# Performance work log

Hardware: AMD Instinct MI355X
Metric: run time of the kernel (lower is better)

Reference implementation:

```python
import jax, jax.numpy as jnp
import numpy as np

B, C, H, Wd = 4, 64, 64, 64


def setup_inputs() -> dict:
    key = jax.random.key(0)
    k1, k2, k3 = jax.random.split(key, 3)
    x = jax.random.normal(k1, (B, C, H, Wd), dtype=jnp.float32)
    W = jax.random.normal(k2, (C, C), dtype=jnp.float32) * (1.0 / np.sqrt(C))
    b = jax.random.normal(k3, (C,), dtype=jnp.float32) * 0.01
    return {"x": x, "W": W, "b": b}


def reference(x, W, b):
    Bz, Cz, Hz, Wz = x.shape
    N = Hz * Wz
    xf = x.reshape(Bz, Cz, N)                      # values [B,C,N]
    # shared 1x1 conv for queries and keys (same module instance in torch)
    qk = jnp.einsum('oc,bcn->bon', W, xf) + b[None, :, None]  # [B,C,N]
    # scores[b,n,m] = sum_c q[b,c,n] * k[b,c,m], scaled by 1/N
    scores = jnp.einsum('bcn,bcm->bnm', qk, qk) / N           # [B,N,N]
    attn = jax.nn.softmax(scores, axis=-1)                    # softmax over m
    # out[b,c,n] = sum_m values[b,c,m] * attn[b,n,m]
    out = jnp.einsum('bcm,bnm->bcn', xf, attn)
    return out.reshape(Bz, Cz, Hz, Wz)
```

## Files before the change

kernel.cpp:

```cpp
#include <hip/hip_runtime.h>
#include <hip/hip_bf16.h>

#define BATCH 4
#define NSP   4096

#define QKSCALE 0.0187675376f

typedef __bf16 bf16x8v __attribute__((ext_vector_type(8)));
typedef __bf16 bf16x4v __attribute__((ext_vector_type(4)));
typedef float  floatx4 __attribute__((ext_vector_type(4)));
typedef float  floatx16 __attribute__((ext_vector_type(16)));
typedef unsigned uivec2 __attribute__((ext_vector_type(2)));

static __device__ __forceinline__ float fast_exp2(float x) {
#if __has_builtin(__builtin_amdgcn_exp2f)
    return __builtin_amdgcn_exp2f(x);
#else
    return exp2f(x);
#endif
}

static __device__ __forceinline__ unsigned pkbf(float a, float b) {
    union { __bf16 h[2]; unsigned u; } x;
    x.h[0] = (__bf16)a; x.h[1] = (__bf16)b;
    return x.u;
}

static __device__ __forceinline__ void plswap(unsigned &a, unsigned &b) {
#if __has_builtin(__builtin_amdgcn_permlane32_swap)
    uivec2 r = __builtin_amdgcn_permlane32_swap(a, b, false, false);
    a = r[0]; b = r[1];
#else
    asm("v_permlane32_swap_b32 %0, %1" : "+v"(a), "+v"(b));
#endif
}

__global__ __launch_bounds__(256) void qk_kernel(const float* __restrict__ x,
                                                 const float* __restrict__ Wm,
                                                 const float* __restrict__ bias,
                                                 __bf16* __restrict__ qkT,
                                                 __bf16* __restrict__ xbf) {
    __shared__ __align__(16) __bf16 xT[64 * 72];

    const int t  = threadIdx.x;
    const int b  = blockIdx.x >> 6;
    const int n0 = (blockIdx.x & 63) << 6;

#pragma unroll
    for (int p = 0; p < 4; ++p) {
        const int c  = p * 16 + (t >> 4);
        const int n4 = (t & 15) * 4;
        const float4 v = *(const float4*)(x + (size_t)(b * 64 + c) * 4096 + n0 + n4);
        xT[(n4 + 0) * 72 + c] = (__bf16)(v.x * QKSCALE);
        xT[(n4 + 1) * 72 + c] = (__bf16)(v.y * QKSCALE);
        xT[(n4 + 2) * 72 + c] = (__bf16)(v.z * QKSCALE);
        xT[(n4 + 3) * 72 + c] = (__bf16)(v.w * QKSCALE);
        bf16x4v xv;
        xv[0] = (__bf16)v.x; xv[1] = (__bf16)v.y; xv[2] = (__bf16)v.z; xv[3] = (__bf16)v.w;
        *(bf16x4v*)(xbf + (size_t)(b * 64 + c) * 4096 + n0 + n4) = xv;
    }
    __syncthreads();

    const int w = t >> 6, lane = t & 63, quad = lane >> 4, l16 = lane & 15;
    const bf16x8v a0 = *(const bf16x8v*)(xT + (w * 16 + l16) * 72 + quad * 8);
    const bf16x8v a1 = *(const bf16x8v*)(xT + (w * 16 + l16) * 72 + 32 + quad * 8);

    floatx4 acc[4];
#pragma unroll
    for (int ot = 0; ot < 4; ++ot) {
        const float* wr = Wm + (ot * 16 + l16) * 64;
        float4 wa = *(const float4*)(wr + quad * 8);
        float4 wb = *(const float4*)(wr + quad * 8 + 4);
        float4 wc = *(const float4*)(wr + 32 + quad * 8);
        float4 wd = *(const float4*)(wr + 32 + quad * 8 + 4);
        bf16x8v b0, b1;
        b0[0]=(__bf16)wa.x; b0[1]=(__bf16)wa.y; b0[2]=(__bf16)wa.z; b0[3]=(__bf16)wa.w;
        b0[4]=(__bf16)wb.x; b0[5]=(__bf16)wb.y; b0[6]=(__bf16)wb.z; b0[7]=(__bf16)wb.w;
        b1[0]=(__bf16)wc.x; b1[1]=(__bf16)wc.y; b1[2]=(__bf16)wc.z; b1[3]=(__bf16)wc.w;
        b1[4]=(__bf16)wd.x; b1[5]=(__bf16)wd.y; b1[6]=(__bf16)wd.z; b1[7]=(__bf16)wd.w;
        acc[ot] = floatx4{0.f, 0.f, 0.f, 0.f};
        acc[ot] = __builtin_amdgcn_mfma_f32_16x16x32_bf16(a0, b0, acc[ot], 0, 0, 0);
        acc[ot] = __builtin_amdgcn_mfma_f32_16x16x32_bf16(a1, b1, acc[ot], 0, 0, 0);
    }
    __syncthreads();

#pragma unroll
    for (int ot = 0; ot < 4; ++ot) {
        const float bo = bias[ot * 16 + l16] * QKSCALE;
#pragma unroll
        for (int r = 0; r < 4; ++r)
            xT[(w * 16 + quad * 4 + r) * 72 + ot * 16 + l16] = (__bf16)(acc[ot][r] + bo);
    }
    __syncthreads();

    const int n = t >> 2, seg = t & 3;
    __bf16* dst = qkT + (size_t)(b * 4096 + n0 + n) * 64 + seg * 16;
    *(bf16x8v*)dst       = *(const bf16x8v*)(xT + n * 72 + seg * 16);
    *(bf16x8v*)(dst + 8) = *(const bf16x8v*)(xT + n * 72 + seg * 16 + 8);
}

template<int SPLIT, int ITERS>
__global__ __launch_bounds__(256, 2) void attn_kernel(const __bf16* __restrict__ xbf,
                                                      const __bf16* __restrict__ qkT,
                                                      __bf16* __restrict__ Opart,
                                                      float* __restrict__ Lpart) {
    __shared__ __align__(16) char smem[66560];
    __bf16* Vlds = (__bf16*)smem;
    float*  Olds = (float*)smem;

    const int t   = threadIdx.x;
    const int blk = blockIdx.x;
    const int xcd = blk & 7;
    const int b   = xcd >> 1;
    const int sub = ((blk >> 3) << 1) | (xcd & 1);
    const int qt  = sub / SPLIT;
    const int s   = sub % SPLIT;
    const int n0  = qt << 8;
    const int pblk = (b * 16 + qt) * SPLIT + s;

    const int w = t >> 6, lane = t & 63, l31 = lane & 31, hi = lane >> 5;

    const __bf16* kgl = qkT + (size_t)b * 4096 * 64;
    const __bf16* vgl = xbf + (size_t)b * 64 * 4096;

    bf16x8v qf[2][4];
#pragma unroll
    for (int qt2 = 0; qt2 < 2; ++qt2) {
        const __bf16* qrow = kgl + (size_t)(n0 + w * 64 + qt2 * 32 + l31) * 64;
#pragma unroll
        for (int kb = 0; kb < 4; ++kb)
            qf[qt2][kb] = *(const bf16x8v*)(qrow + kb * 16 + hi * 8);
    }

    floatx16 oacc[2][2] = {};
    float rs[2] = {0.f, 0.f};

    const int c0    = t >> 3;
    const int col8  = t & 7;
    const int slot0 = ((col8 ^ (c0 & 7)) * 8);
    uint4 vst0, vst1;
    auto stage_load = [&](int m0) {
        vst0 = *(const uint4*)(vgl + (size_t)c0 * 4096 + m0 + col8 * 8);
        vst1 = *(const uint4*)(vgl + (size_t)(c0 + 32) * 4096 + m0 + col8 * 8);
    };
    auto stage_write = [&](int buf) {
        __bf16* vd = Vlds + buf * 4096;
        *(uint4*)(vd + c0 * 64 + slot0)        = vst0;
        *(uint4*)(vd + (c0 + 32) * 64 + slot0) = vst1;
    };

    const int mbase = s * (64 * ITERS);
    stage_load(mbase);
    stage_write(0);
    int cur = 0;

    for (int it = 0; it < ITERS; ++it) {
        const int m0 = mbase + (it << 6);
        if (it + 1 < ITERS) stage_load(m0 + 64);
        __syncthreads();
        const __bf16* Vc = Vlds + cur * 4096;

#pragma unroll
        for (int mt = 0; mt < 2; ++mt) {
            bf16x8v kf[4];
#pragma unroll
            for (int kb = 0; kb < 4; ++kb)
                kf[kb] = *(const bf16x8v*)(kgl + (size_t)(m0 + mt * 32 + l31) * 64 + kb * 16 + hi * 8);

            bf16x8v vf[2][2];
#pragma unroll
            for (int ct = 0; ct < 2; ++ct)
#pragma unroll
                for (int ks = 0; ks < 2; ++ks) {
                    const int c  = ct * 32 + l31;
                    const int sl = ((mt * 4 + ks * 2 + hi) ^ (c & 7)) * 8;
                    vf[ct][ks] = *(const bf16x8v*)(Vc + c * 64 + sl);
                }

#pragma unroll
            for (int qt2 = 0; qt2 < 2; ++qt2) {
                floatx16 acc = {};
#pragma unroll
                for (int kb = 0; kb < 4; ++kb)
                    acc = __builtin_amdgcn_mfma_f32_32x32x16_bf16(kf[kb], qf[qt2][kb], acc, 0, 0, 0);

                float p[16];
                float sum = 0.f;
#pragma unroll
                for (int i = 0; i < 16; ++i) { p[i] = fast_exp2(acc[i]); sum += p[i]; }
                rs[qt2] += sum;

                unsigned wd0 = pkbf(p[0],  p[1]),  wd1 = pkbf(p[2],  p[3]);
                unsigned wd2 = pkbf(p[4],  p[5]),  wd3 = pkbf(p[6],  p[7]);
                unsigned wd4 = pkbf(p[8],  p[9]),  wd5 = pkbf(p[10], p[11]);
                unsigned wd6 = pkbf(p[12], p[13]), wd7 = pkbf(p[14], p[15]);
                plswap(wd0, wd2);
                plswap(wd1, wd3);
                plswap(wd4, wd6);
                plswap(wd5, wd7);
                union { unsigned u[4]; bf16x8v v; } pb0, pb1;
                pb0.u[0] = wd0; pb0.u[1] = wd1; pb0.u[2] = wd2; pb0.u[3] = wd3;
                pb1.u[0] = wd4; pb1.u[1] = wd5; pb1.u[2] = wd6; pb1.u[3] = wd7;

#pragma unroll
                for (int ct = 0; ct < 2; ++ct) {
                    oacc[qt2][ct] = __builtin_amdgcn_mfma_f32_32x32x16_bf16(vf[ct][0], pb0.v, oacc[qt2][ct], 0, 0, 0);
                    oacc[qt2][ct] = __builtin_amdgcn_mfma_f32_32x32x16_bf16(vf[ct][1], pb1.v, oacc[qt2][ct], 0, 0, 0);
                }
            }
        }

        if (it + 1 < ITERS) stage_write(cur ^ 1);
        cur ^= 1;
    }

#pragma unroll
    for (int qt2 = 0; qt2 < 2; ++qt2) {
        float v = rs[qt2] + __shfl_xor(rs[qt2], 32, 64);
        if (lane < 32)
            Lpart[(size_t)pblk * 256 + w * 64 + qt2 * 32 + l31] = v;
    }

    __syncthreads();

#pragma unroll
    for (int qt2 = 0; qt2 < 2; ++qt2)
#pragma unroll
        for (int ct = 0; ct < 2; ++ct)
#pragma unroll
            for (int r = 0; r < 16; ++r) {
                const int c = ct * 32 + (r & 3) + 8 * (r >> 2) + 4 * hi;
                Olds[c * 260 + w * 64 + qt2 * 32 + l31] = oacc[qt2][ct][r];
            }
    __syncthreads();

    const int c = t >> 2, qb = (t & 3) * 64;
#pragma unroll
    for (int i = 0; i < 8; ++i) {
        floatx4 v0 = *(const floatx4*)(Olds + c * 260 + qb + i * 8);
        floatx4 v1 = *(const floatx4*)(Olds + c * 260 + qb + i * 8 + 4);
        bf16x8v pk;
        pk[0]=(__bf16)v0[0]; pk[1]=(__bf16)v0[1]; pk[2]=(__bf16)v0[2]; pk[3]=(__bf16)v0[3];
        pk[4]=(__bf16)v1[0]; pk[5]=(__bf16)v1[1]; pk[6]=(__bf16)v1[2]; pk[7]=(__bf16)v1[3];
        *(bf16x8v*)(Opart + (size_t)pblk * 16384 + c * 256 + qb + i * 8) = pk;
    }
}

template<int SPLIT>
__global__ __launch_bounds__(256) void reduce_kernel(const __bf16* __restrict__ Opart,
                                                     const float* __restrict__ Lpart,
                                                     float* __restrict__ out) {
    const int blk = blockIdx.x;
    const int bq = blk >> 3, cq = blk & 7;
    const int b = bq >> 4, qt = bq & 15;
    const int t = threadIdx.x;
    const int c  = cq * 8 + (t >> 5);
    const int q8 = (t & 31) * 8;

    float l[8] = {0.f,0.f,0.f,0.f,0.f,0.f,0.f,0.f};
#pragma unroll
    for (int s = 0; s < SPLIT; ++s) {
        const float* lp = Lpart + ((size_t)bq * SPLIT + s) * 256 + q8;
        float4 u = *(const float4*)lp;
        float4 v = *(const float4*)(lp + 4);
        l[0]+=u.x; l[1]+=u.y; l[2]+=u.z; l[3]+=u.w;
        l[4]+=v.x; l[5]+=v.y; l[6]+=v.z; l[7]+=v.w;
    }
    float a[8] = {0.f,0.f,0.f,0.f,0.f,0.f,0.f,0.f};
#pragma unroll
    for (int s = 0; s < SPLIT; ++s) {
        bf16x8v v = *(const bf16x8v*)(Opart + ((size_t)bq * SPLIT + s) * 16384 + c * 256 + q8);
#pragma unroll
        for (int k = 0; k < 8; ++k) a[k] += (float)v[k];
    }
    float* op = out + (size_t)(b * 64 + c) * 4096 + qt * 256 + q8;
    float4 o0, o1;
    o0.x = a[0]/l[0]; o0.y = a[1]/l[1]; o0.z = a[2]/l[2]; o0.w = a[3]/l[3];
    o1.x = a[4]/l[4]; o1.y = a[5]/l[5]; o1.z = a[6]/l[6]; o1.w = a[7]/l[7];
    *(float4*)op       = o0;
    *(float4*)(op + 4) = o1;
}

extern "C" void kernel_launch(void* const* d_in, const int* in_sizes, int n_in,
                              void* d_out, int out_size, void* d_ws, size_t ws_size,
                              hipStream_t stream) {
    const float* x    = (const float*)d_in[0];
    const float* Wm   = (const float*)d_in[1];
    const float* bias = (const float*)d_in[2];
    float* out = (float*)d_out;

    char* ws = (char*)d_ws;
    __bf16* qkT = (__bf16*)ws;
    __bf16* xbf = (__bf16*)(ws + 2097152);

    qk_kernel<<<BATCH * (NSP / 64), 256, 0, stream>>>(x, Wm, bias, qkT, xbf);

    const size_t HEAD = 2097152 + 2097152;
    const size_t needBig = HEAD + (size_t)512 * 16384 * 2 + (size_t)512 * 256 * 4;
    if (ws_size >= needBig) {
        __bf16* Opart = (__bf16*)(ws + HEAD);
        float*  Lpart = (float*)(ws + HEAD + (size_t)512 * 16384 * 2);
        attn_kernel<8, 8><<<BATCH * 16 * 8, 256, 0, stream>>>(xbf, qkT, Opart, Lpart);
        reduce_kernel<8><<<512, 256, 0, stream>>>(Opart, Lpart, out);
    } else {
        __bf16* Opart = (__bf16*)(ws + HEAD);
        float*  Lpart = (float*)(ws + HEAD + (size_t)256 * 16384 * 2);
        attn_kernel<4, 16><<<BATCH * 16 * 4, 256, 0, stream>>>(xbf, qkT, Opart, Lpart);
        reduce_kernel<4><<<512, 256, 0, stream>>>(Opart, Lpart, out);
    }
}
```

Baseline: 102.6 us.

## Stage K tiles through double-buffered LDS and raise wave priority during MFMA

K rows used in the score MFMA are now staged cooperatively into a swizzled, double-buffered LDS region alongside V, instead of each wave reading them directly from global memory. All four waves share the same K tile, so this replaces redundant global/L2 reads with one coalesced load per block plus LDS reads. The compute section is also wrapped in s_setprio to favour MFMA issue over other waves. The cost is more LDS traffic and extra registers for the prefetch staging, which could affect occupancy at two blocks per CU.

```diff
diff --git a/kernel.cpp b/kernel.cpp
--- a/kernel.cpp
+++ b/kernel.cpp
@@ -105,7 +105,8 @@
                                                       __bf16* __restrict__ Opart,
                                                       float* __restrict__ Lpart) {
     __shared__ __align__(16) char smem[66560];
-    __bf16* Vlds = (__bf16*)smem;
+    __bf16* Klds = (__bf16*)smem;
+    __bf16* Vlds = (__bf16*)(smem + 16384);
     float*  Olds = (float*)smem;
 
     const int t   = threadIdx.x;
@@ -135,18 +136,23 @@
     floatx16 oacc[2][2] = {};
     float rs[2] = {0.f, 0.f};
 
-    const int c0    = t >> 3;
-    const int col8  = t & 7;
-    const int slot0 = ((col8 ^ (c0 & 7)) * 8);
-    uint4 vst0, vst1;
+    const int srow = t >> 3;
+    const int scol = t & 7;
+    const int slot = ((scol ^ (srow & 7)) * 8);
+    uint4 kst0, kst1, vst0, vst1;
     auto stage_load = [&](int m0) {
-        vst0 = *(const uint4*)(vgl + (size_t)c0 * 4096 + m0 + col8 * 8);
-        vst1 = *(const uint4*)(vgl + (size_t)(c0 + 32) * 4096 + m0 + col8 * 8);
+        kst0 = *(const uint4*)(kgl + (size_t)(m0 + srow) * 64 + scol * 8);
+        kst1 = *(const uint4*)(kgl + (size_t)(m0 + srow + 32) * 64 + scol * 8);
+        vst0 = *(const uint4*)(vgl + (size_t)srow * 4096 + m0 + scol * 8);
+        vst1 = *(const uint4*)(vgl + (size_t)(srow + 32) * 4096 + m0 + scol * 8);
     };
     auto stage_write = [&](int buf) {
+        __bf16* kd = Klds + buf * 4096;
         __bf16* vd = Vlds + buf * 4096;
-        *(uint4*)(vd + c0 * 64 + slot0)        = vst0;
-        *(uint4*)(vd + (c0 + 32) * 64 + slot0) = vst1;
+        *(uint4*)(kd + srow * 64 + slot)        = kst0;
+        *(uint4*)(kd + (srow + 32) * 64 + slot) = kst1;
+        *(uint4*)(vd + srow * 64 + slot)        = vst0;
+        *(uint4*)(vd + (srow + 32) * 64 + slot) = vst1;
     };
 
     const int mbase = s * (64 * ITERS);
@@ -155,27 +161,27 @@
     int cur = 0;
 
     for (int it = 0; it < ITERS; ++it) {
-        const int m0 = mbase + (it << 6);
-        if (it + 1 < ITERS) stage_load(m0 + 64);
+        if (it + 1 < ITERS) stage_load(mbase + ((it + 1) << 6));
         __syncthreads();
+        const __bf16* Kc = Klds + cur * 4096;
         const __bf16* Vc = Vlds + cur * 4096;
 
+        __builtin_amdgcn_s_setprio(1);
 #pragma unroll
         for (int mt = 0; mt < 2; ++mt) {
             bf16x8v kf[4];
 #pragma unroll
             for (int kb = 0; kb < 4; ++kb)
-                kf[kb] = *(const bf16x8v*)(kgl + (size_t)(m0 + mt * 32 + l31) * 64 + kb * 16 + hi * 8);
+                kf[kb] = *(const bf16x8v*)(Kc + (mt * 32 + l31) * 64 +
+                                           (((kb * 2 + hi) ^ (l31 & 7)) * 8));
 
             bf16x8v vf[2][2];
 #pragma unroll
             for (int ct = 0; ct < 2; ++ct)
 #pragma unroll
-                for (int ks = 0; ks < 2; ++ks) {
-                    const int c  = ct * 32 + l31;
-                    const int sl = ((mt * 4 + ks * 2 + hi) ^ (c & 7)) * 8;
-                    vf[ct][ks] = *(const bf16x8v*)(Vc + c * 64 + sl);
-                }
+                for (int ks = 0; ks < 2; ++ks)
+                    vf[ct][ks] = *(const bf16x8v*)(Vc + (ct * 32 + l31) * 64 +
+                                                   (((mt * 4 + ks * 2 + hi) ^ (l31 & 7)) * 8));
 
 #pragma unroll
             for (int qt2 = 0; qt2 < 2; ++qt2) {
@@ -209,6 +215,7 @@
                 }
             }
         }
+        __builtin_amdgcn_s_setprio(0);
 
         if (it + 1 < ITERS) stage_write(cur ^ 1);
         cur ^= 1;
```

Result: faster. 98.37 us (-4.1%).
